# Optimization experiments

Measured on AMD Instinct MI355X. Metric: run time of the kernel, lower is better.

The kernel has to match this reference:

```python
import jax, jax.numpy as jnp
import numpy as np

NUM_EMBEDDINGS = 1024
EMBEDDING_DIM = 512
COMMITMENT_COST = 0.25


def setup_inputs() -> dict:
    key = jax.random.key(0)
    k1, k2 = jax.random.split(key)
    inputs = jax.random.normal(k1, (128, 512, EMBEDDING_DIM), dtype=jnp.float32)
    # torch init: uniform_(-1/K, 1/K)
    emb_weight = jax.random.uniform(
        k2, (NUM_EMBEDDINGS, EMBEDDING_DIM), dtype=jnp.float32,
        minval=-1.0 / NUM_EMBEDDINGS, maxval=1.0 / NUM_EMBEDDINGS)
    return {"inputs": inputs, "emb_weight": emb_weight}


def reference(inputs, emb_weight):
    K, D = emb_weight.shape
    flat = inputs.reshape(-1, D)  # [N, D]
    # squared euclidean distances to every code: [N, K]
    distances = (jnp.sum(flat * flat, axis=1, keepdims=True)
                 + jnp.sum(emb_weight * emb_weight, axis=1)
                 - 2.0 * jnp.matmul(flat, emb_weight.T))
    encoding_indices = jnp.argmin(distances, axis=1)  # [N]
    encodings = jax.nn.one_hot(encoding_indices, K, dtype=inputs.dtype)  # [N, K]
    # matmul(one_hot, W) == gather; use gather (same math, efficient form)
    quantized = jnp.take(emb_weight, encoding_indices, axis=0).reshape(inputs.shape)
    e_latent_loss = jnp.mean((jax.lax.stop_gradient(quantized) - inputs) ** 2)
    q_latent_loss = jnp.mean((quantized - jax.lax.stop_gradient(inputs)) ** 2)
    loss = q_latent_loss + COMMITMENT_COST * e_latent_loss
    # straight-through estimator
    quantized_st = inputs + jax.lax.stop_gradient(quantized - inputs)
    avg_probs = jnp.mean(encodings, axis=0)
    perplexity = jnp.exp(-jnp.sum(avg_probs * jnp.log(avg_probs + 1e-10)))
    return (loss, quantized_st, perplexity, encodings)
```

## Files before the change

### kernel.cpp

```cpp
#include <hip/hip_runtime.h>
#include <stdint.h>

typedef unsigned short u16;
typedef unsigned long long u64;
using short8 = __attribute__((ext_vector_type(8))) short;
using f32x16 = __attribute__((ext_vector_type(16))) float;

#define NROWS 65536
#define DIM   512
#define KC    1024

#define GLOBAL_AS __attribute__((address_space(1)))
#define LDS_AS    __attribute__((address_space(3)))

__device__ __forceinline__ void gload_lds16(const void* g, void* l) {
  __builtin_amdgcn_global_load_lds((const GLOBAL_AS uint32_t*)g,
                                   (LDS_AS uint32_t*)l, 16, 0, 0);
}

__device__ __forceinline__ u16 f2bf(float f) {
  unsigned u = __float_as_uint(f);
  return (u16)((u + 0x7fffu + ((u >> 16) & 1u)) >> 16);
}

__global__ __launch_bounds__(256) void wprep_kernel(const float* __restrict__ W,
                                                    short8* __restrict__ WhT8,
                                                    float* __restrict__ wnorm,
                                                    int* __restrict__ counts,
                                                    double* __restrict__ sums) {
  if (blockIdx.x == 0) {
    for (int k = threadIdx.x; k < KC; k += 256) counts[k] = 0;
    if (threadIdx.x < 2) sums[threadIdx.x] = 0.0;
  }
  int code = blockIdx.x * 4 + (threadIdx.x >> 6);
  int l = threadIdx.x & 63;
  const float* wr = W + (size_t)code * DIM + l * 8;
  float4 v0 = *(const float4*)wr;
  float4 v1 = *(const float4*)(wr + 4);
  float s = v0.x * v0.x + v0.y * v0.y + v0.z * v0.z + v0.w * v0.w
          + v1.x * v1.x + v1.y * v1.y + v1.z * v1.z + v1.w * v1.w;
  short8 pk;
  pk[0] = (short)f2bf(v0.x); pk[1] = (short)f2bf(v0.y);
  pk[2] = (short)f2bf(v0.z); pk[3] = (short)f2bf(v0.w);
  pk[4] = (short)f2bf(v1.x); pk[5] = (short)f2bf(v1.y);
  pk[6] = (short)f2bf(v1.z); pk[7] = (short)f2bf(v1.w);
  WhT8[(size_t)(code >> 5) * 2048 + (l >> 1) * 64 + (l & 1) * 32 + (code & 31)] = pk;
#pragma unroll
  for (int off = 32; off; off >>= 1) s += __shfl_xor(s, off, 64);
  if (l == 0) wnorm[code] = s;
}

__global__ __launch_bounds__(256)
__attribute__((amdgpu_waves_per_eu(2, 2))) void mm_kernel(
    const float* __restrict__ X, const float* __restrict__ W,
    const u16* __restrict__ WhTf, const float* __restrict__ wnorm,
    int* __restrict__ counts, double* __restrict__ sums,
    float* __restrict__ quant, float* __restrict__ encf) {
  __shared__ __align__(16) u16 BsU[2][16384];
  __shared__ int rowk[128];
  __shared__ double sdbl[4];
  const int t = threadIdx.x;
  const int w = t >> 6, l = t & 63;
  const int r = l & 31, h = l >> 5;
  const int row0 = blockIdx.x * 128;

#pragma unroll
  for (int i = 0; i < 8; ++i)
    gload_lds16(WhTf + i * 2048 + t * 8, &BsU[0][i * 2048 + t * 8]);

  const float* Xr = X + (size_t)(row0 + w * 32 + r) * DIM + h * 8;
  short8 aF[32];
  double xacc = 0.0;
#pragma unroll
  for (int s = 0; s < 32; ++s) {
    float4 v0 = *(const float4*)(Xr + s * 16);
    float4 v1 = *(const float4*)(Xr + s * 16 + 4);
    xacc += (double)v0.x * v0.x + (double)v0.y * v0.y + (double)v0.z * v0.z + (double)v0.w * v0.w
          + (double)v1.x * v1.x + (double)v1.y * v1.y + (double)v1.z * v1.z + (double)v1.w * v1.w;
    short8 pk;
    pk[0] = (short)f2bf(v0.x); pk[1] = (short)f2bf(v0.y);
    pk[2] = (short)f2bf(v0.z); pk[3] = (short)f2bf(v0.w);
    pk[4] = (short)f2bf(v1.x); pk[5] = (short)f2bf(v1.y);
    pk[6] = (short)f2bf(v1.z); pk[7] = (short)f2bf(v1.w);
    aF[s] = pk;
  }
#pragma unroll
  for (int off = 32; off; off >>= 1) xacc += __shfl_xor(xacc, off, 64);
  if (l == 0) atomicAdd(&sums[0], xacc);

  unsigned best_[16];
#pragma unroll
  for (int q = 0; q < 16; ++q) best_[q] = 0xFFFFFFFFu;

  float4* encz = (float4*)(encf + (size_t)row0 * KC);
  const float4 zero4 = {0.f, 0.f, 0.f, 0.f};

  __syncthreads();

  for (int kt = 0; kt < 32; ++kt) {
    const int buf = kt & 1;
    if (kt < 31) {
      const u16* src = WhTf + (size_t)(kt + 1) * 16384;
#pragma unroll
      for (int i = 0; i < 8; ++i)
        gload_lds16(src + i * 2048 + t * 8, &BsU[buf ^ 1][i * 2048 + t * 8]);
    }
#pragma unroll
    for (int j = 0; j < 4; ++j) encz[kt * 1024 + j * 256 + t] = zero4;

    const u16* bufp = &BsU[buf][l * 8];
    f32x16 acc_e = {}, acc_o = {};
#pragma unroll
    for (int ks = 0; ks < 32; ++ks) {
      short8 bv = *(const short8*)&bufp[ks * 512];
      if (ks & 1)
        acc_o = __builtin_amdgcn_mfma_f32_32x32x16_bf16(aF[ks], bv, acc_o, 0, 0, 0);
      else
        acc_e = __builtin_amdgcn_mfma_f32_32x32x16_bf16(aF[ks], bv, acc_e, 0, 0, 0);
    }
    float wn = wnorm[kt * 32 + r];
    unsigned col = (unsigned)(kt * 32 + r);
#pragma unroll
    for (int q = 0; q < 16; ++q) {
      float sc = fmaf(-2.0f, acc_e[q] + acc_o[q], wn);
      unsigned u_ = __float_as_uint(sc);
      unsigned key = (u_ & 0x80000000u) ? ~u_ : (u_ | 0x80000000u);
      best_[q] = min(best_[q], (key & 0xFFFFFC00u) | col);
    }
    __syncthreads();
  }

  double local = 0.0;
#pragma unroll
  for (int q = 0; q < 16; ++q) {
    unsigned pb = best_[q];
#pragma unroll
    for (int off = 16; off; off >>= 1)
      pb = min(pb, (unsigned)__shfl_xor((int)pb, off, 32));
    if (r == 0) {
      int rit = w * 32 + (q & 3) + 8 * (q >> 2) + 4 * h;
      int k = (int)(pb & 1023u);
      rowk[rit] = k;
      atomicAdd(&counts[k], 1);
      unsigned key = (pb & 0xFFFFFC00u) | 0x200u;
      unsigned uu = (key & 0x80000000u) ? (key ^ 0x80000000u) : ~key;
      local += (double)__uint_as_float(uu);
    }
  }
  {
    double o32 = __shfl(local, 32, 64);
    if (l == 0) sdbl[w] = local + o32;
  }
  __syncthreads();
  if (t == 0) atomicAdd(&sums[1], sdbl[0] + sdbl[1] + sdbl[2] + sdbl[3]);

  for (int j = 0; j < 32; ++j) {
    int rit = w * 32 + j;
    int k = rowk[rit];
    size_t row = (size_t)(row0 + rit);
    float4 wv0 = *(const float4*)&W[(size_t)k * DIM + l * 8];
    float4 wv1 = *(const float4*)&W[(size_t)k * DIM + l * 8 + 4];
    float* dst = quant + row * DIM + l * 8;
    dst[0] = wv0.x; dst[1] = wv0.y; dst[2] = wv0.z; dst[3] = wv0.w;
    dst[4] = wv1.x; dst[5] = wv1.y; dst[6] = wv1.z; dst[7] = wv1.w;
    if (l == 0) encf[row * KC + k] = 1.0f;
  }
}

__global__ __launch_bounds__(256) void finalize_kernel(
    const int* __restrict__ counts, const double* __restrict__ sums,
    float* __restrict__ out_loss, float* __restrict__ out_perp) {
  __shared__ float red[4];
  int t = threadIdx.x;
  float h = 0.f;
  for (int k = t; k < KC; k += 256) {
    float p = (float)counts[k] / (float)NROWS;
    h -= p * logf(p + 1e-10f);
  }
#pragma unroll
  for (int off = 32; off; off >>= 1) h += __shfl_xor(h, off, 64);
  if ((t & 63) == 0) red[t >> 6] = h;
  __syncthreads();
  if (t == 0) {
    float H = red[0] + red[1] + red[2] + red[3];
    *out_perp = expf(H);
    double m = (sums[0] + sums[1]) / (double)((long long)NROWS * DIM);
    *out_loss = (float)(1.25 * m);
  }
}

extern "C" void kernel_launch(void* const* d_in, const int* in_sizes, int n_in,
                              void* d_out, int out_size, void* d_ws, size_t ws_size,
                              hipStream_t stream) {
  const float* X = (const float*)d_in[0];
  const float* W = (const float*)d_in[1];
  float* out = (float*)d_out;
  char* ws = (char*)d_ws;

  float* out_loss = out;
  float* quant    = out + 1;
  float* out_perp = out + 1 + NROWS * DIM;
  float* encf     = out + 2 + NROWS * DIM;

  short8* WhT8   = (short8*)ws;
  float*  wnorm  = (float*)(ws + (1040u << 10));
  int*    counts = (int*)(ws + (1040u << 10) + 4096);
  double* sums   = (double*)(ws + (1040u << 10) + 8192);

  wprep_kernel<<<KC / 4, 256, 0, stream>>>(W, WhT8, wnorm, counts, sums);
  mm_kernel<<<NROWS / 128, 256, 0, stream>>>(X, W, (const u16*)WhT8, wnorm,
                                             counts, sums, quant, encf);
  finalize_kernel<<<1, 256, 0, stream>>>(counts, sums, out_loss, out_perp);
}
```

Baseline: 193.2 us.

## Use nontemporal loads/stores, aligned quantized writes, and finer barrier waits

Loads X and stores the zeroed one-hot rows through nontemporal loads and stores. The quantized output starts at offset 1 in the output buffer, so it is misaligned; the copy now shifts elements so each vector store lands on a 16-byte boundary, and the edge elements are written with scalar stores. Replaces __syncthreads with an explicit s_waitcnt vmcnt(4) plus s_barrier so the prefetch of the next LDS tile can stay in flight. The vmcnt(4) count assumes a specific number of outstanding memory operations, which risks a race if the compiler schedules them differently.

```diff
diff --git a/kernel.cpp b/kernel.cpp
--- a/kernel.cpp
+++ b/kernel.cpp
@@ -5,6 +5,7 @@
 typedef unsigned long long u64;
 using short8 = __attribute__((ext_vector_type(8))) short;
 using f32x16 = __attribute__((ext_vector_type(16))) float;
+using f32x4v = __attribute__((ext_vector_type(4))) float;
 
 #define NROWS 65536
 #define DIM   512
@@ -21,6 +22,13 @@
 __device__ __forceinline__ u16 f2bf(float f) {
   unsigned u = __float_as_uint(f);
   return (u16)((u + 0x7fffu + ((u >> 16) & 1u)) >> 16);
+}
+
+__device__ __forceinline__ f32x4v ntload4(const float* p) {
+  return __builtin_nontemporal_load((const f32x4v*)p);
+}
+__device__ __forceinline__ void ntstore4(float* p, f32x4v v) {
+  __builtin_nontemporal_store(v, (f32x4v*)p);
 }
 
 __global__ __launch_bounds__(256) void wprep_kernel(const float* __restrict__ W,
@@ -55,7 +63,7 @@
     const float* __restrict__ X, const float* __restrict__ W,
     const u16* __restrict__ WhTf, const float* __restrict__ wnorm,
     int* __restrict__ counts, double* __restrict__ sums,
-    float* __restrict__ quant, float* __restrict__ encf) {
+    float* __restrict__ out, float* __restrict__ encf) {
   __shared__ __align__(16) u16 BsU[2][16384];
   __shared__ int rowk[128];
   __shared__ double sdbl[4];
@@ -73,15 +81,15 @@
   double xacc = 0.0;
 #pragma unroll
   for (int s = 0; s < 32; ++s) {
-    float4 v0 = *(const float4*)(Xr + s * 16);
-    float4 v1 = *(const float4*)(Xr + s * 16 + 4);
-    xacc += (double)v0.x * v0.x + (double)v0.y * v0.y + (double)v0.z * v0.z + (double)v0.w * v0.w
-          + (double)v1.x * v1.x + (double)v1.y * v1.y + (double)v1.z * v1.z + (double)v1.w * v1.w;
+    f32x4v v0 = ntload4(Xr + s * 16);
+    f32x4v v1 = ntload4(Xr + s * 16 + 4);
+    xacc += (double)v0[0] * v0[0] + (double)v0[1] * v0[1] + (double)v0[2] * v0[2] + (double)v0[3] * v0[3]
+          + (double)v1[0] * v1[0] + (double)v1[1] * v1[1] + (double)v1[2] * v1[2] + (double)v1[3] * v1[3];
     short8 pk;
-    pk[0] = (short)f2bf(v0.x); pk[1] = (short)f2bf(v0.y);
-    pk[2] = (short)f2bf(v0.z); pk[3] = (short)f2bf(v0.w);
-    pk[4] = (short)f2bf(v1.x); pk[5] = (short)f2bf(v1.y);
-    pk[6] = (short)f2bf(v1.z); pk[7] = (short)f2bf(v1.w);
+    pk[0] = (short)f2bf(v0[0]); pk[1] = (short)f2bf(v0[1]);
+    pk[2] = (short)f2bf(v0[2]); pk[3] = (short)f2bf(v0[3]);
+    pk[4] = (short)f2bf(v1[0]); pk[5] = (short)f2bf(v1[1]);
+    pk[6] = (short)f2bf(v1[2]); pk[7] = (short)f2bf(v1[3]);
     aF[s] = pk;
   }
 #pragma unroll
@@ -92,10 +100,12 @@
 #pragma unroll
   for (int q = 0; q < 16; ++q) best_[q] = 0xFFFFFFFFu;
 
-  float4* encz = (float4*)(encf + (size_t)row0 * KC);
-  const float4 zero4 = {0.f, 0.f, 0.f, 0.f};
-
-  __syncthreads();
+  f32x4v* encz = (f32x4v*)(encf + (size_t)row0 * KC);
+  const f32x4v zero4 = {0.f, 0.f, 0.f, 0.f};
+
+  asm volatile("s_waitcnt vmcnt(0)" ::: "memory");
+  __builtin_amdgcn_s_barrier();
+  __builtin_amdgcn_sched_barrier(0);
 
   for (int kt = 0; kt < 32; ++kt) {
     const int buf = kt & 1;
@@ -106,7 +116,8 @@
         gload_lds16(src + i * 2048 + t * 8, &BsU[buf ^ 1][i * 2048 + t * 8]);
     }
 #pragma unroll
-    for (int j = 0; j < 4; ++j) encz[kt * 1024 + j * 256 + t] = zero4;
+    for (int j = 0; j < 4; ++j)
+      __builtin_nontemporal_store(zero4, &encz[kt * 1024 + j * 256 + t]);
 
     const u16* bufp = &BsU[buf][l * 8];
     f32x16 acc_e = {}, acc_o = {};
@@ -127,7 +138,9 @@
       unsigned key = (u_ & 0x80000000u) ? ~u_ : (u_ | 0x80000000u);
       best_[q] = min(best_[q], (key & 0xFFFFFC00u) | col);
     }
-    __syncthreads();
+    asm volatile("s_waitcnt vmcnt(4)" ::: "memory");
+    __builtin_amdgcn_s_barrier();
+    __builtin_amdgcn_sched_barrier(0);
   }
 
   double local = 0.0;
@@ -157,13 +170,24 @@
   for (int j = 0; j < 32; ++j) {
     int rit = w * 32 + j;
     int k = rowk[rit];
-    size_t row = (size_t)(row0 + rit);
-    float4 wv0 = *(const float4*)&W[(size_t)k * DIM + l * 8];
-    float4 wv1 = *(const float4*)&W[(size_t)k * DIM + l * 8 + 4];
-    float* dst = quant + row * DIM + l * 8;
-    dst[0] = wv0.x; dst[1] = wv0.y; dst[2] = wv0.z; dst[3] = wv0.w;
-    dst[4] = wv1.x; dst[5] = wv1.y; dst[6] = wv1.z; dst[7] = wv1.w;
-    if (l == 0) encf[row * KC + k] = 1.0f;
+    const float* Wr = W + (size_t)k * DIM;
+    size_t ob = (size_t)(row0 + rit) * DIM;
+    {
+      f32x4v cm = *(const f32x4v*)(Wr + 4 * l);
+      f32x4v c1 = *(const f32x4v*)(Wr + 4 * l + 4);
+      f32x4v sv = {cm[3], c1[0], c1[1], c1[2]};
+      ntstore4(out + ob + 4 + 4 * l, sv);
+    }
+    if (l <= 62) {
+      int m = l + 64;
+      f32x4v dm = *(const f32x4v*)(Wr + 4 * m);
+      f32x4v d1 = *(const f32x4v*)(Wr + 4 * m + 4);
+      f32x4v sv = {dm[3], d1[0], d1[1], d1[2]};
+      ntstore4(out + ob + 4 + 4 * m, sv);
+    }
+    if (l < 3) out[ob + 1 + l] = Wr[l];
+    if (l == 3) out[ob + 512] = Wr[511];
+    if (l == 4) encf[(size_t)(row0 + rit) * KC + k] = 1.0f;
   }
 }
 
@@ -198,7 +222,6 @@
   char* ws = (char*)d_ws;
 
   float* out_loss = out;
-  float* quant    = out + 1;
   float* out_perp = out + 1 + NROWS * DIM;
   float* encf     = out + 2 + NROWS * DIM;
 
@@ -209,6 +232,6 @@
 
   wprep_kernel<<<KC / 4, 256, 0, stream>>>(W, WhT8, wnorm, counts, sums);
   mm_kernel<<<NROWS / 128, 256, 0, stream>>>(X, W, (const u16*)WhT8, wnorm,
-                                             counts, sums, quant, encf);
+                                             counts, sums, out, encf);
   finalize_kernel<<<1, 256, 0, stream>>>(counts, sums, out_loss, out_perp);
 }
```

After: 180.4 us. 6.6% less time.
